# Kernel optimization log

Hardware: AMD Instinct MI355X
Metric: run time of the kernel (lower is better)

## Reference

```python
import jax, jax.numpy as jnp
import numpy as np

SEQ, BATCH, IN, HID = 2048, 16, 512, 512
QMAX = 127.0  # 8-bit narrow-range signed


def round_ste(x):
    # straight-through rounding (brevitas FloatToIntImplType.ROUND with STE)
    return x + jax.lax.stop_gradient(jnp.round(x) - x)


def weight_fake_quant(w, threshold):
    # scalar per-tensor scale = max|W| over concatenated [W_ri; W_rh], narrow-range int8
    s = threshold / QMAX
    return jnp.clip(round_ste(w / s), -QMAX, QMAX) * s


def act_fake_quant(x):
    # CONST scaling over [-1, 1], signed narrow-range int8 -> scale 1/127
    return jnp.clip(round_ste(x * QMAX), -QMAX, QMAX) / QMAX


def rnn_direction(inputs, w_ri, w_rh, b, reverse):
    threshold = jnp.maximum(jnp.max(jnp.abs(w_ri)), jnp.max(jnp.abs(w_rh)))
    q_ri = weight_fake_quant(w_ri, threshold)
    q_rh = weight_fake_quant(w_rh, threshold)
    xs = jnp.flip(inputs, 0) if reverse else inputs
    state0 = jnp.zeros((inputs.shape[1], w_rh.shape[0]), inputs.dtype)
    state0 = act_fake_quant(jnp.clip(state0, -1.0, 1.0))  # quant_input(state)

    def step(state, x_t):
        x_q = act_fake_quant(jnp.clip(x_t, -1.0, 1.0))  # QuantHardTanh on input
        gate = x_q @ q_ri + state @ q_rh + b            # [batch, hid]
        h = act_fake_quant(jnp.tanh(gate))              # QuantTanh
        return h, h

    _, outs = jax.lax.scan(step, state0, xs)            # [seq, batch, hid]
    return jnp.flip(outs, 0) if reverse else outs


def setup_inputs() -> dict:
    key = jax.random.key(0)
    ks = jax.random.split(key, 7)
    stdv = 1.0 / np.sqrt(HID)
    u = lambda k, shape: jax.random.uniform(k, shape, jnp.float32, -stdv, stdv)
    return {
        "inputs": jax.random.normal(ks[0], (SEQ, BATCH, IN), jnp.float32),
        "w_ri_f": u(ks[1], (IN, HID)),
        "w_rh_f": u(ks[2], (HID, HID)),
        "b_f": u(ks[3], (HID,)),
        "w_ri_b": u(ks[4], (IN, HID)),
        "w_rh_b": u(ks[5], (HID, HID)),
        "b_b": u(ks[6], (HID,)),
    }


def reference(inputs, w_ri_f, w_rh_f, b_f, w_ri_b, w_rh_b, b_b):
    out_f = rnn_direction(inputs, w_ri_f, w_rh_f, b_f, reverse=False)
    out_b = rnn_direction(inputs, w_ri_b, w_rh_b, b_b, reverse=True)
    return jnp.concatenate([out_f, out_b], axis=-1)  # [seq, batch, 2*hid]
```

## Files before the change

kernel.cpp:

```cpp
#include <hip/hip_runtime.h>
#include <stdint.h>

typedef int i32x4 __attribute__((ext_vector_type(4)));

#define TWO_LOG2E 2.8853900817779268f

#define WS_XQ_OFF   4096
#define XQ_BYTES    ((size_t)32768 * 512)
#define WRIT_BYTES  ((size_t)1024 * 512)
#define WRHT_BYTES  ((size_t)2 * 512 * 512)

static __device__ __forceinline__ int dot4(int a, int b, int c) {
#if __has_builtin(__builtin_amdgcn_sdot4)
    return __builtin_amdgcn_sdot4(a, b, c, false);
#else
    int r = c;
    r += (int)(signed char)(a) * (int)(signed char)(b);
    r += (int)(signed char)(a >> 8) * (int)(signed char)(b >> 8);
    r += (int)(signed char)(a >> 16) * (int)(signed char)(b >> 16);
    r += (int)(signed char)(a >> 24) * (int)(signed char)(b >> 24);
    return r;
#endif
}

__global__ __launch_bounds__(256) void k_absmax(const float* __restrict__ wri_f,
                                                const float* __restrict__ wrh_f,
                                                const float* __restrict__ wri_b,
                                                const float* __restrict__ wrh_b,
                                                unsigned* thrbits) {
    int dir = blockIdx.y;
    const float* a = dir ? wri_b : wri_f;
    const float* c = dir ? wrh_b : wrh_f;
    float m = 0.f;
    for (int i = blockIdx.x * 256 + threadIdx.x; i < 512 * 512; i += gridDim.x * 256) {
        m = fmaxf(m, fabsf(a[i]));
        m = fmaxf(m, fabsf(c[i]));
    }
    __shared__ float red[256];
    red[threadIdx.x] = m;
    __syncthreads();
    for (int s = 128; s > 0; s >>= 1) {
        if (threadIdx.x < s) red[threadIdx.x] = fmaxf(red[threadIdx.x], red[threadIdx.x + s]);
        __syncthreads();
    }
    if (threadIdx.x == 0) atomicMax(&thrbits[dir], __float_as_uint(red[0]));
}

__global__ __launch_bounds__(256) void k_quant_w(const float* __restrict__ wri_f,
                                                 const float* __restrict__ wrh_f,
                                                 const float* __restrict__ wri_b,
                                                 const float* __restrict__ wrh_b,
                                                 const unsigned* __restrict__ thrbits,
                                                 signed char* __restrict__ writ,
                                                 signed char* __restrict__ wrht) {
    int id = blockIdx.x;
    int dir = id & 1;
    int which = (id >> 1) & 1;
    int tile = id >> 2;
    int ti = tile >> 3, tj = tile & 7;
    const float* src = which ? (dir ? wrh_b : wrh_f) : (dir ? wri_b : wri_f);
    signed char* dst = which ? (wrht + (size_t)dir * 512 * 512) : (writ + (size_t)dir * 512 * 512);
    float s = __uint_as_float(thrbits[dir]) / 127.0f;
    __shared__ signed char t8[64][68];
    int tx = threadIdx.x & 63, ty = threadIdx.x >> 6;
    int i0 = ti * 64, j0 = tj * 64;
#pragma unroll
    for (int r = 0; r < 16; ++r) {
        int il = r * 4 + ty;
        float w = src[(size_t)(i0 + il) * 512 + j0 + tx];
        float q = rintf(w / s);
        q = fminf(fmaxf(q, -127.f), 127.f);
        t8[il][tx] = (signed char)(int)q;
    }
    __syncthreads();
#pragma unroll
    for (int r = 0; r < 16; ++r) {
        int jl = r * 4 + ty;
        dst[(size_t)(j0 + jl) * 512 + i0 + tx] = t8[tx][jl];
    }
}

__global__ __launch_bounds__(256) void k_quant_x(const float* __restrict__ x,
                                                 signed char* __restrict__ xq) {
    int i = blockIdx.x * 256 + threadIdx.x;
    float4 v = ((const float4*)x)[i];
    int q0 = (int)rintf(fminf(fmaxf(v.x, -1.f), 1.f) * 127.f);
    int q1 = (int)rintf(fminf(fmaxf(v.y, -1.f), 1.f) * 127.f);
    int q2 = (int)rintf(fminf(fmaxf(v.z, -1.f), 1.f) * 127.f);
    int q3 = (int)rintf(fminf(fmaxf(v.w, -1.f), 1.f) * 127.f);
    ((int*)xq)[i] = (q0 & 255) | ((q1 & 255) << 8) | ((q2 & 255) << 16) | ((q3 & 255) << 24);
}

__global__ __launch_bounds__(256, 2) void k_gemm_xif(const signed char* __restrict__ xq,
                                                     const signed char* __restrict__ writ,
                                                     const float* __restrict__ b_f,
                                                     const float* __restrict__ b_b,
                                                     const unsigned* __restrict__ thrbits,
                                                     float* __restrict__ out) {
    int bid = blockIdx.x;
    int mt8 = bid >> 3;
    int nt8 = bid & 7;
    int w = threadIdx.x >> 6, lane = threadIdx.x & 63;
    int l15 = lane & 15, q = lane >> 4;
    int M0 = mt8 * 128 + (w >> 1) * 64;
    int N0 = nt8 * 128 + (w & 1) * 64;
    int dir = N0 >> 9;
    float thr = __uint_as_float(thrbits[dir]);
    float gs2 = thr * (TWO_LOG2E / (127.f * 127.f));
    const float* bp = dir ? b_b : b_f;
    float bi2[4];
#pragma unroll
    for (int nt = 0; nt < 4; ++nt)
        bi2[nt] = bp[(N0 & 511) + nt * 16 + l15] * TWO_LOG2E;

    i32x4 acc[4][4];
#pragma unroll
    for (int mt = 0; mt < 4; ++mt)
#pragma unroll
        for (int nt = 0; nt < 4; ++nt)
            acc[mt][nt] = (i32x4){0, 0, 0, 0};

#pragma unroll
    for (int kb = 0; kb < 8; ++kb) {
        i32x4 af[4], bf[4];
#pragma unroll
        for (int mt = 0; mt < 4; ++mt)
            af[mt] = *(const i32x4*)(xq + (size_t)(M0 + mt * 16 + l15) * 512 + kb * 64 + q * 16);
#pragma unroll
        for (int nt = 0; nt < 4; ++nt)
            bf[nt] = *(const i32x4*)(writ + (size_t)(N0 + nt * 16 + l15) * 512 + kb * 64 + q * 16);
#pragma unroll
        for (int mt = 0; mt < 4; ++mt)
#pragma unroll
            for (int nt = 0; nt < 4; ++nt)
                acc[mt][nt] = __builtin_amdgcn_mfma_i32_16x16x64_i8(af[mt], bf[nt], acc[mt][nt], 0, 0, 0);
    }
#pragma unroll
    for (int mt = 0; mt < 4; ++mt)
#pragma unroll
        for (int nt = 0; nt < 4; ++nt)
#pragma unroll
            for (int r = 0; r < 4; ++r) {
                int row = M0 + mt * 16 + q * 4 + r;
                int col = N0 + nt * 16 + l15;
                out[(size_t)row * 1024 + col] = fmaf((float)acc[mt][nt][r], gs2, bi2[nt]);
            }
}

__global__ __launch_bounds__(512, 2) void k_rnn(const signed char* __restrict__ wrht,
                                                const unsigned* __restrict__ thrbits,
                                                float* __restrict__ out) {
    int bid = blockIdx.x;
    int dir = bid >> 4, batch = bid & 15;
    int n = threadIdx.x;
    float thr = __uint_as_float(thrbits[dir]);
    float gs2 = thr * (TWO_LOG2E / (127.f * 127.f));
    const signed char* wq = wrht + (size_t)dir * 512 * 512 + (size_t)n * 512;

    i32x4 w[32];
#pragma unroll
    for (int i = 0; i < 32; ++i)
        w[i] = *(const i32x4*)(wq + i * 16);

    __shared__ __align__(16) signed char st[2][512];
    if (threadIdx.x < 256) ((int*)st)[threadIdx.x] = 0;
    __syncthreads();

    int t0 = dir ? 2047 : 0;
    const long long rowstride = (long long)(dir ? -1 : 1) * 16 * 1024;
    float* prow = out + (size_t)t0 * 16 * 1024 + (size_t)batch * 1024 + (size_t)dir * 512 + n;

    float xi = *prow;
    int pp = 0;
    for (int step = 0; step < 2048; ++step) {
        float* pnext = prow + ((step + 1 < 2048) ? rowstride : 0);
        float xin = *pnext;

        int acc0 = 0, acc1 = 0, acc2 = 0, acc3 = 0;
#pragma unroll
        for (int kb = 0; kb < 32; ++kb) {
            i32x4 s4 = *(const i32x4*)&st[pp][kb * 16];
            acc0 = dot4(w[kb][0], s4[0], acc0);
            acc1 = dot4(w[kb][1], s4[1], acc1);
            acc2 = dot4(w[kb][2], s4[2], acc2);
            acc3 = dot4(w[kb][3], s4[3], acc3);
        }
        int acc = (acc0 + acc1) + (acc2 + acc3);

        float arg = fmaf((float)acc, gs2, xi);
        float e = __builtin_amdgcn_exp2f(arg);
        float r = __builtin_amdgcn_rcpf(1.0f + e);
        float h127 = rintf(fmaf(r, -254.0f, 127.0f));
        *prow = h127 * (1.0f / 127.0f);
        st[pp ^ 1][n] = (signed char)(int)h127;

        xi = xin;
        prow = pnext;
        asm volatile("s_waitcnt lgkmcnt(0)" ::: "memory");
        __builtin_amdgcn_s_barrier();
        __builtin_amdgcn_sched_barrier(0);
        pp ^= 1;
    }
}

extern "C" void kernel_launch(void* const* d_in, const int* in_sizes, int n_in,
                              void* d_out, int out_size, void* d_ws, size_t ws_size,
                              hipStream_t stream) {
    const float* x     = (const float*)d_in[0];
    const float* wri_f = (const float*)d_in[1];
    const float* wrh_f = (const float*)d_in[2];
    const float* b_f   = (const float*)d_in[3];
    const float* wri_b = (const float*)d_in[4];
    const float* wrh_b = (const float*)d_in[5];
    const float* b_b   = (const float*)d_in[6];
    float* out = (float*)d_out;
    char* ws = (char*)d_ws;

    size_t need = WS_XQ_OFF + XQ_BYTES + WRIT_BYTES + WRHT_BYTES;
    if (ws_size < need) return;

    unsigned* thrbits = (unsigned*)ws;
    signed char* xq   = (signed char*)(ws + WS_XQ_OFF);
    signed char* writ = xq + XQ_BYTES;
    signed char* wrht = writ + WRIT_BYTES;

    hipMemsetAsync(thrbits, 0, 8, stream);
    k_absmax<<<dim3(64, 2), 256, 0, stream>>>(wri_f, wrh_f, wri_b, wrh_b, thrbits);
    k_quant_w<<<256, 256, 0, stream>>>(wri_f, wrh_f, wri_b, wrh_b, thrbits, writ, wrht);
    k_quant_x<<<16384, 256, 0, stream>>>(x, xq);
    k_gemm_xif<<<2048, 256, 0, stream>>>(xq, writ, b_f, b_b, thrbits, out);
    k_rnn<<<32, 512, 0, stream>>>(wrht, thrbits, out);
}
```

Before: 1.622 ms.

## Split recurrent dot products across 8 lanes with shuffle reduction in RNN kernel

The recurrent kernel now runs 1024 threads per block. Each group of 8 lanes owns 4 output columns, and each lane covers a 64-wide K slice, with partial sums combined through xor-shuffles. The hidden state in shared memory uses a padded layout of 8 rows of 72 bytes, so the split K reads avoid bank conflicts. Lanes 0-3 of each group write the output row and lanes 4-7 write the new state, splitting the stores. This cuts the serial dot4 chain per thread from 128 to 64 and the per-thread weight registers from 128 to 64 VGPRs, at the cost of shuffle rounds and a larger barrier per timestep.

Result: slower. 4.947 ms (+204.9%).

```diff
diff --git a/kernel.cpp b/kernel.cpp
--- a/kernel.cpp
+++ b/kernel.cpp
@@ -147,28 +147,37 @@
             }
 }
 
-__global__ __launch_bounds__(512, 2) void k_rnn(const signed char* __restrict__ wrht,
-                                                const unsigned* __restrict__ thrbits,
-                                                float* __restrict__ out) {
+__global__ __launch_bounds__(1024, 1) void k_rnn(const signed char* __restrict__ wrht,
+                                                 const unsigned* __restrict__ thrbits,
+                                                 float* __restrict__ out) {
     int bid = blockIdx.x;
     int dir = bid >> 4, batch = bid & 15;
-    int n = threadIdx.x;
+    int tid = threadIdx.x;
+    int g = tid >> 3;
+    int s = tid & 7;
+    int cmy = 4 * g + (s & 3);
     float thr = __uint_as_float(thrbits[dir]);
     float gs2 = thr * (TWO_LOG2E / (127.f * 127.f));
-    const signed char* wq = wrht + (size_t)dir * 512 * 512 + (size_t)n * 512;
-
-    i32x4 w[32];
-#pragma unroll
-    for (int i = 0; i < 32; ++i)
-        w[i] = *(const i32x4*)(wq + i * 16);
-
-    __shared__ __align__(16) signed char st[2][512];
-    if (threadIdx.x < 256) ((int*)st)[threadIdx.x] = 0;
+    const signed char* wq = wrht + (size_t)dir * 512 * 512;
+
+    i32x4 w[4][4];
+#pragma unroll
+    for (int i = 0; i < 4; ++i)
+#pragma unroll
+        for (int j = 0; j < 4; ++j)
+            w[i][j] = *(const i32x4*)(wq + (size_t)(4 * g + i) * 512 + s * 64 + j * 16);
+
+    __shared__ __align__(16) signed char st[2][8 * 72];
+    for (int i = tid; i < 2 * 8 * 72 / 4; i += 1024) ((int*)st)[i] = 0;
     __syncthreads();
+
+    const signed char* rdp0 = &st[0][s * 72];
+    const signed char* rdp1 = &st[1][s * 72];
+    int woff = (cmy >> 6) * 72 + (cmy & 63);
 
     int t0 = dir ? 2047 : 0;
     const long long rowstride = (long long)(dir ? -1 : 1) * 16 * 1024;
-    float* prow = out + (size_t)t0 * 16 * 1024 + (size_t)batch * 1024 + (size_t)dir * 512 + n;
+    float* prow = out + (size_t)t0 * 16 * 1024 + (size_t)batch * 1024 + (size_t)dir * 512 + cmy;
 
     float xi = *prow;
     int pp = 0;
@@ -176,23 +185,36 @@
         float* pnext = prow + ((step + 1 < 2048) ? rowstride : 0);
         float xin = *pnext;
 
-        int acc0 = 0, acc1 = 0, acc2 = 0, acc3 = 0;
-#pragma unroll
-        for (int kb = 0; kb < 32; ++kb) {
-            i32x4 s4 = *(const i32x4*)&st[pp][kb * 16];
-            acc0 = dot4(w[kb][0], s4[0], acc0);
-            acc1 = dot4(w[kb][1], s4[1], acc1);
-            acc2 = dot4(w[kb][2], s4[2], acc2);
-            acc3 = dot4(w[kb][3], s4[3], acc3);
+        const signed char* sp = pp ? rdp1 : rdp0;
+        int a0 = 0, a1 = 0, a2 = 0, a3 = 0;
+#pragma unroll
+        for (int j = 0; j < 4; ++j) {
+            i32x4 s4 = *(const i32x4*)(sp + j * 16);
+            a0 = dot4(w[0][j][0], s4[0], a0); a0 = dot4(w[0][j][1], s4[1], a0);
+            a0 = dot4(w[0][j][2], s4[2], a0); a0 = dot4(w[0][j][3], s4[3], a0);
+            a1 = dot4(w[1][j][0], s4[0], a1); a1 = dot4(w[1][j][1], s4[1], a1);
+            a1 = dot4(w[1][j][2], s4[2], a1); a1 = dot4(w[1][j][3], s4[3], a1);
+            a2 = dot4(w[2][j][0], s4[0], a2); a2 = dot4(w[2][j][1], s4[1], a2);
+            a2 = dot4(w[2][j][2], s4[2], a2); a2 = dot4(w[2][j][3], s4[3], a2);
+            a3 = dot4(w[3][j][0], s4[0], a3); a3 = dot4(w[3][j][1], s4[1], a3);
+            a3 = dot4(w[3][j][2], s4[2], a3); a3 = dot4(w[3][j][3], s4[3], a3);
         }
-        int acc = (acc0 + acc1) + (acc2 + acc3);
-
-        float arg = fmaf((float)acc, gs2, xi);
+        a0 += __shfl_xor(a0, 1); a1 += __shfl_xor(a1, 1);
+        a2 += __shfl_xor(a2, 1); a3 += __shfl_xor(a3, 1);
+        a0 += __shfl_xor(a0, 2); a1 += __shfl_xor(a1, 2);
+        a2 += __shfl_xor(a2, 2); a3 += __shfl_xor(a3, 2);
+        a0 += __shfl_xor(a0, 4); a1 += __shfl_xor(a1, 4);
+        a2 += __shfl_xor(a2, 4); a3 += __shfl_xor(a3, 4);
+        int t01 = (s & 1) ? a1 : a0;
+        int t23 = (s & 1) ? a3 : a2;
+        int afin = (s & 2) ? t23 : t01;
+
+        float arg = fmaf((float)afin, gs2, xi);
         float e = __builtin_amdgcn_exp2f(arg);
         float r = __builtin_amdgcn_rcpf(1.0f + e);
         float h127 = rintf(fmaf(r, -254.0f, 127.0f));
-        *prow = h127 * (1.0f / 127.0f);
-        st[pp ^ 1][n] = (signed char)(int)h127;
+        if (s < 4) *prow = h127 * (1.0f / 127.0f);
+        else st[pp ^ 1][woff] = (signed char)(int)h127;
 
         xi = xin;
         prow = pnext;
@@ -229,5 +251,5 @@
     k_quant_w<<<256, 256, 0, stream>>>(wri_f, wrh_f, wri_b, wrh_b, thrbits, writ, wrht);
     k_quant_x<<<16384, 256, 0, stream>>>(x, xq);
     k_gemm_xif<<<2048, 256, 0, stream>>>(xq, writ, b_f, b_b, thrbits, out);
-    k_rnn<<<32, 512, 0, stream>>>(wrht, thrbits, out);
-}
+    k_rnn<<<32, 1024, 0, stream>>>(wrht, thrbits, out);
+}
```
